# Optimization experiments

Hardware: AMD Instinct MI355X
Metric: run time of the kernel (lower is better)

The kernel has to match this reference:

```python
import jax, jax.numpy as jnp
import numpy as np

NEG_BIG = 1e20


def setup_inputs() -> dict:
    key = jax.random.key(0)
    k1, k2, k3 = jax.random.split(key, 3)
    B, Tenc, Tdec, D = 8, 2048, 512, 1024
    enc = jax.random.normal(k1, (B, Tenc, D), dtype=jnp.float32)
    dec = jax.random.normal(k2, (B, Tdec, D), dtype=jnp.float32)
    enc_mask = jax.random.randint(k3, (B, Tenc), 0, 2, dtype=jnp.int32)
    # guarantee at least one valid position per row to keep softmax well-defined
    enc_mask = enc_mask.at[:, 0].set(1)
    return {"enc": enc, "enc_mask": enc_mask, "dec": dec}


def reference(enc, enc_mask, dec):
    # dropout=0 and identity transforms -> enc_trans = enc, dec_trans = dec
    mask = enc_mask.astype(enc.dtype)  # (B, Tenc)
    # raw scores: sum_d dec[b,u,d] * enc[b,t,d] -> (B, Tenc, Tdec)
    raw = jnp.einsum('btd,bud->btu', enc, dec)
    raw = raw - (1.0 - mask)[:, :, None] * NEG_BIG
    scores = jax.nn.softmax(raw, axis=1)  # softmax over Tenc
    # context: sum_t scores[b,t,u] * enc[b,t,d] -> (B, Tdec, D)
    context = jnp.einsum('btu,btd->bud', scores, enc)
    return context, scores
```

## Files before the change

### kernel.cpp

```cpp
#include <hip/hip_runtime.h>
#include <math.h>

#define BATCH 8
#define TENC 2048
#define TDEC 512
#define DIM 1024
#define NEG_BIG 1e20f

typedef __attribute__((ext_vector_type(8))) short short8;
typedef __attribute__((ext_vector_type(4))) float f32x4;
typedef unsigned short ushort_t;

__device__ __forceinline__ unsigned int bf16rn(float x) {
    unsigned int u = __float_as_uint(x);
    return (u + 0x7FFFu + ((u >> 16) & 1u)) >> 16;
}
__device__ __forceinline__ float bf16f(unsigned int b) {
    return __uint_as_float(b << 16);
}
__device__ __forceinline__ void split2(float x, unsigned int& h, unsigned int& l) {
    h = bf16rn(x);
    l = bf16rn(x - bf16f(h));
}

#define GLOAD16(g, l)                                                        \
    __builtin_amdgcn_global_load_lds(                                        \
        (const __attribute__((address_space(1))) unsigned int*)(g),          \
        (__attribute__((address_space(3))) unsigned int*)(l), 16, 0, 0)


__global__ __launch_bounds__(256) void prep_enc(
    const float* __restrict__ enc, ushort_t* __restrict__ encH,
    ushort_t* __restrict__ encL, ushort_t* __restrict__ encT)
{
    __shared__ ushort_t T[64][72];

    const int b  = blockIdx.z;
    const int t0 = blockIdx.y * 64;
    const int d0 = blockIdx.x * 64;
    const int tid = threadIdx.x;

    const int tr = tid >> 4;
    const int dc = (tid & 15) * 4;

    const float* E = enc + (size_t)b * TENC * DIM;

#pragma unroll
    for (int i = 0; i < 4; ++i) {
        const int t = t0 + tr + 16 * i;
        float4 x = *(const float4*)&E[(size_t)t * DIM + d0 + dc];
        float xs[4] = {x.x, x.y, x.z, x.w};
        unsigned int h[4], l[4];
#pragma unroll
        for (int j = 0; j < 4; ++j) split2(xs[j], h[j], l[j]);
        ushort_t* ph = &encH[((size_t)b * TENC + t) * DIM + d0 + dc];
        ushort_t* pl = &encL[((size_t)b * TENC + t) * DIM + d0 + dc];
        *(uint2*)ph = make_uint2(h[0] | (h[1] << 16), h[2] | (h[3] << 16));
        *(uint2*)pl = make_uint2(l[0] | (l[1] << 16), l[2] | (l[3] << 16));
        const int tloc = tr + 16 * i;
#pragma unroll
        for (int j = 0; j < 4; ++j) T[dc + j][tloc] = (ushort_t)h[j];
    }
    __syncthreads();

    const int dr = tid >> 2;
    const int tc = (tid & 3) * 16;
    short8 v0 = *(const short8*)&T[dr][tc];
    short8 v1 = *(const short8*)&T[dr][tc + 8];
    ushort_t* out = &encT[((size_t)b * DIM + d0 + dr) * TENC + t0 + tc];
    *(short8*)out = v0;
    *(short8*)(out + 8) = v1;
}

__global__ __launch_bounds__(256) void prep_dec(
    const float* __restrict__ dec, ushort_t* __restrict__ decH,
    ushort_t* __restrict__ decL)
{
    const size_t i4 = (size_t)blockIdx.x * 256 + threadIdx.x;
    float4 x = *(const float4*)(dec + i4 * 4);
    float xs[4] = {x.x, x.y, x.z, x.w};
    unsigned int h[4], l[4];
#pragma unroll
    for (int j = 0; j < 4; ++j) split2(xs[j], h[j], l[j]);
    *(uint2*)(decH + i4 * 4) = make_uint2(h[0] | (h[1] << 16), h[2] | (h[3] << 16));
    *(uint2*)(decL + i4 * 4) = make_uint2(l[0] | (l[1] << 16), l[2] | (l[3] << 16));
}

__global__ __launch_bounds__(256) void gemm1_lds(
    const ushort_t* __restrict__ encH, const ushort_t* __restrict__ encL,
    const ushort_t* __restrict__ decH, const ushort_t* __restrict__ decL,
    const int* __restrict__ mask, float* __restrict__ raw,
    float* __restrict__ pm, float* __restrict__ ps)
{
    __shared__ __align__(16) ushort_t Ah[128 * 32];
    __shared__ __align__(16) ushort_t Al[128 * 32];
    __shared__ __align__(16) ushort_t Bh[128 * 32];
    __shared__ __align__(16) ushort_t Bl[128 * 32];
    __shared__ float smx[4][68];
    __shared__ float ssx[4][68];

    const int b  = blockIdx.z;
    const int m0 = blockIdx.y * 128;
    const int n0 = blockIdx.x * 128;
    const int tid = threadIdx.x;

    const int lane = tid & 63;
    const int w    = tid >> 6;
    const int wm   = (w & 1) * 64;
    const int wn   = (w >> 1) * 64;
    const int lr   = lane & 15;
    const int q    = lane >> 4;

    const int srow   = lane & 15;
    const int schunk = (lane >> 4) * 8;

    const int fa = wm * 32 + q * 128 + lr * 8;
    const int fb = wn * 32 + q * 128 + lr * 8;

    const ushort_t* AH = encH + (size_t)b * TENC * DIM;
    const ushort_t* AL = encL + (size_t)b * TENC * DIM;
    const ushort_t* BH = decH + (size_t)b * TDEC * DIM;
    const ushort_t* BL = decL + (size_t)b * TDEC * DIM;
    float* C = raw + (size_t)b * TENC * TDEC;

    f32x4 acc[4][4] = {};

    for (int k0 = 0; k0 < DIM; k0 += 32) {
        __syncthreads();
#pragma unroll
        for (int q2 = 0; q2 < 2; ++q2) {
            const int rg  = w * 2 + q2;
            const int row = rg * 16 + srow;
            const size_t ga = (size_t)(m0 + row) * DIM + k0 + schunk;
            const size_t gb = (size_t)(n0 + row) * DIM + k0 + schunk;
            GLOAD16(AH + ga, &Ah[rg * 512]);
            GLOAD16(AL + ga, &Al[rg * 512]);
            GLOAD16(BH + gb, &Bh[rg * 512]);
            GLOAD16(BL + gb, &Bl[rg * 512]);
        }
        __syncthreads();

        short8 ah[4], al[4], bh[4], bl[4];
#pragma unroll
        for (int i = 0; i < 4; ++i) {
            ah[i] = *(const short8*)&Ah[fa + i * 512];
            al[i] = *(const short8*)&Al[fa + i * 512];
            bh[i] = *(const short8*)&Bh[fb + i * 512];
            bl[i] = *(const short8*)&Bl[fb + i * 512];
        }
#pragma unroll
        for (int i = 0; i < 4; ++i)
#pragma unroll
            for (int j = 0; j < 4; ++j) {
                acc[i][j] = __builtin_amdgcn_mfma_f32_16x16x32_bf16(ah[i], bh[j], acc[i][j], 0, 0, 0);
                acc[i][j] = __builtin_amdgcn_mfma_f32_16x16x32_bf16(ah[i], bl[j], acc[i][j], 0, 0, 0);
                acc[i][j] = __builtin_amdgcn_mfma_f32_16x16x32_bf16(al[i], bh[j], acc[i][j], 0, 0, 0);
            }
    }

    float mkv[4][4];
#pragma unroll
    for (int i = 0; i < 4; ++i)
#pragma unroll
        for (int rr = 0; rr < 4; ++rr) {
            const int t = m0 + wm + i * 16 + q * 4 + rr;
            mkv[i][rr] = (mask[b * TENC + t] == 0) ? NEG_BIG : 0.0f;
        }

    float cm[4] = {-INFINITY, -INFINITY, -INFINITY, -INFINITY};
    float cs[4] = {0.f, 0.f, 0.f, 0.f};
#pragma unroll
    for (int i = 0; i < 4; ++i)
#pragma unroll
        for (int rr = 0; rr < 4; ++rr) {
            const int t = m0 + wm + i * 16 + q * 4 + rr;
#pragma unroll
            for (int j = 0; j < 4; ++j) {
                const int u = n0 + wn + j * 16 + lr;
                const float v = acc[i][j][rr] - mkv[i][rr];
                C[(size_t)t * TDEC + u] = v;
                cm[j] = fmaxf(cm[j], v);
            }
        }
#pragma unroll
    for (int i = 0; i < 4; ++i)
#pragma unroll
        for (int rr = 0; rr < 4; ++rr)
#pragma unroll
            for (int j = 0; j < 4; ++j)
                cs[j] += __expf(acc[i][j][rr] - mkv[i][rr] - cm[j]);

#pragma unroll
    for (int j = 0; j < 4; ++j) {
#pragma unroll
        for (int d = 16; d < 64; d <<= 1) {
            float om = __shfl_xor(cm[j], d, 64);
            float os = __shfl_xor(cs[j], d, 64);
            float mn = fmaxf(cm[j], om);
            cs[j] = cs[j] * __expf(cm[j] - mn) + os * __expf(om - mn);
            cm[j] = mn;
        }
    }

    if (q == 0) {
#pragma unroll
        for (int j = 0; j < 4; ++j) {
            smx[w][j * 16 + lr] = cm[j];
            ssx[w][j * 16 + lr] = cs[j];
        }
    }
    __syncthreads();
    if (tid < 128) {
        const int col = tid;
        const int wp  = (col >> 6) * 2;
        const int ci  = col & 63;
        const float m1 = smx[wp][ci],     s1 = ssx[wp][ci];
        const float m2 = smx[wp + 1][ci], s2 = ssx[wp + 1][ci];
        const float M = fmaxf(m1, m2);
        const float S = s1 * __expf(m1 - M) + s2 * __expf(m2 - M);
        const int idx = b * TDEC + n0 + col;
        const int tb  = m0 >> 7;
        pm[(size_t)tb * (BATCH * TDEC) + idx] = M;
        ps[(size_t)tb * (BATCH * TDEC) + idx] = S;
    }
}

__global__ __launch_bounds__(256) void colstat2(
    const float* __restrict__ pm, const float* __restrict__ ps,
    float* __restrict__ colM, float* __restrict__ colI)
{
    const int idx = blockIdx.x * 256 + threadIdx.x;
    float M = -INFINITY;
#pragma unroll
    for (int z = 0; z < 16; ++z)
        M = fmaxf(M, pm[(size_t)z * (BATCH * TDEC) + idx]);
    float s = 0.0f;
#pragma unroll
    for (int z = 0; z < 16; ++z)
        s += ps[(size_t)z * (BATCH * TDEC) + idx] *
             __expf(pm[(size_t)z * (BATCH * TDEC) + idx] - M);
    colM[idx] = M;
    colI[idx] = 1.0f / s;
}

__global__ __launch_bounds__(256) void norm_kernel(
    float* __restrict__ S, const float* __restrict__ colM,
    const float* __restrict__ colI, ushort_t* __restrict__ scoresT)
{
    __shared__ ushort_t T[64][72];

    const int b  = blockIdx.z;
    const int t0 = blockIdx.x * 64;
    const int u0 = blockIdx.y * 64;
    const int tid = threadIdx.x;

    const int tr  = tid >> 4;
    const int ucl = (tid & 15) * 4;

    float4 M4 = *(const float4*)&colM[b * TDEC + u0 + ucl];
    float4 I4 = *(const float4*)&colI[b * TDEC + u0 + ucl];

    float* base = S + (size_t)b * TENC * TDEC;

#pragma unroll
    for (int i = 0; i < 4; ++i) {
        const int t = t0 + tr + 16 * i;
        float4 x = *(const float4*)&base[(size_t)t * TDEC + u0 + ucl];
        float4 p;
        p.x = __expf(x.x - M4.x) * I4.x;
        p.y = __expf(x.y - M4.y) * I4.y;
        p.z = __expf(x.z - M4.z) * I4.z;
        p.w = __expf(x.w - M4.w) * I4.w;
        *(float4*)&base[(size_t)t * TDEC + u0 + ucl] = p;
        const int tloc = tr + 16 * i;
        T[ucl + 0][tloc] = (ushort_t)bf16rn(p.x);
        T[ucl + 1][tloc] = (ushort_t)bf16rn(p.y);
        T[ucl + 2][tloc] = (ushort_t)bf16rn(p.z);
        T[ucl + 3][tloc] = (ushort_t)bf16rn(p.w);
    }
    __syncthreads();

    const int ur = tid >> 2;
    const int tc = (tid & 3) * 16;
    short8 v0 = *(const short8*)&T[ur][tc];
    short8 v1 = *(const short8*)&T[ur][tc + 8];
    ushort_t* out = &scoresT[((size_t)b * TDEC + u0 + ur) * TENC + t0 + tc];
    *(short8*)out = v0;
    *(short8*)(out + 8) = v1;
}

__global__ __launch_bounds__(256) void gemm2_lds(
    const ushort_t* __restrict__ scoresT, const ushort_t* __restrict__ encT,
    float* __restrict__ p0, float* __restrict__ p1)
{
    __shared__ __align__(16) ushort_t Ah[128 * 32];
    __shared__ __align__(16) ushort_t Bh[128 * 32];

    const int b  = blockIdx.z >> 1;
    const int ks = blockIdx.z & 1;
    const int m0 = blockIdx.y * 128;
    const int n0 = blockIdx.x * 128;
    const int tid = threadIdx.x;

    const int lane = tid & 63;
    const int w    = tid >> 6;
    const int wm   = (w & 1) * 64;
    const int wn   = (w >> 1) * 64;
    const int lr   = lane & 15;
    const int q    = lane >> 4;

    const int srow   = lane & 15;
    const int schunk = (lane >> 4) * 8;
    const int fa = wm * 32 + q * 128 + lr * 8;
    const int fb = wn * 32 + q * 128 + lr * 8;

    const ushort_t* A = scoresT + (size_t)b * TDEC * TENC;
    const ushort_t* B = encT    + (size_t)b * DIM * TENC;
    float* P = (ks ? p1 : p0) + (size_t)b * TDEC * DIM;

    const int kbeg = ks * (TENC / 2);
    const int kend = kbeg + TENC / 2;

    f32x4 acc[4][4] = {};

    for (int k0 = kbeg; k0 < kend; k0 += 32) {
        __syncthreads();
#pragma unroll
        for (int q2 = 0; q2 < 2; ++q2) {
            const int rg  = w * 2 + q2;
            const int row = rg * 16 + srow;
            GLOAD16(A + (size_t)(m0 + row) * TENC + k0 + schunk, &Ah[rg * 512]);
            GLOAD16(B + (size_t)(n0 + row) * TENC + k0 + schunk, &Bh[rg * 512]);
        }
        __syncthreads();

        short8 ah[4], bh[4];
#pragma unroll
        for (int i = 0; i < 4; ++i) {
            ah[i] = *(const short8*)&Ah[fa + i * 512];
            bh[i] = *(const short8*)&Bh[fb + i * 512];
        }
#pragma unroll
        for (int i = 0; i < 4; ++i)
#pragma unroll
            for (int j = 0; j < 4; ++j)
                acc[i][j] = __builtin_amdgcn_mfma_f32_16x16x32_bf16(ah[i], bh[j], acc[i][j], 0, 0, 0);
    }

#pragma unroll
    for (int i = 0; i < 4; ++i)
#pragma unroll
        for (int rr = 0; rr < 4; ++rr) {
            const int u = m0 + wm + i * 16 + q * 4 + rr;
#pragma unroll
            for (int j = 0; j < 4; ++j) {
                const int d = n0 + wn + j * 16 + lr;
                P[(size_t)u * DIM + d] = acc[i][j][rr];
            }
        }
}

__global__ __launch_bounds__(256) void reduce_ctx(
    const float* __restrict__ p0, const float* __restrict__ p1,
    float* __restrict__ ctx)
{
    const size_t i4 = ((size_t)blockIdx.x * 256 + threadIdx.x) * 4;
    float4 a = *(const float4*)(p0 + i4);
    float4 b = *(const float4*)(p1 + i4);
    float4 o;
    o.x = a.x + b.x; o.y = a.y + b.y; o.z = a.z + b.z; o.w = a.w + b.w;
    *(float4*)(ctx + i4) = o;
}


__device__ __forceinline__ void store8(ushort_t* ph, ushort_t* pl,
                                       float4 x0, float4 x1) {
    float xs[8] = {x0.x, x0.y, x0.z, x0.w, x1.x, x1.y, x1.z, x1.w};
    short8 hv, lv;
#pragma unroll
    for (int i = 0; i < 8; ++i) {
        unsigned int h, l;
        split2(xs[i], h, l);
        hv[i] = (short)h;
        lv[i] = (short)l;
    }
    *(short8*)ph = hv;
    *(short8*)pl = lv;
}

__device__ __forceinline__ void wr4(ushort_t* ph, ushort_t* pl, const float* x) {
    unsigned int h[4], l[4];
#pragma unroll
    for (int i = 0; i < 4; ++i) split2(x[i], h[i], l[i]);
    *(uint2*)ph = make_uint2(h[0] | (h[1] << 16), h[2] | (h[3] << 16));
    *(uint2*)pl = make_uint2(l[0] | (l[1] << 16), l[2] | (l[3] << 16));
}

__device__ __forceinline__ short8 frag8B(const ushort_t* p) {
    union { short8 v; uint2 u[2]; } f;
    f.u[0] = *(const uint2*)p;
    f.u[1] = *(const uint2*)(p + 4);
    return f.v;
}

__global__ __launch_bounds__(256) void gemm1_mfma(
    const float* __restrict__ enc, const float* __restrict__ dec,
    const int* __restrict__ mask, float* __restrict__ raw)
{
    __shared__ __align__(16) ushort_t Ah[128 * 32];
    __shared__ __align__(16) ushort_t Al[128 * 32];
    __shared__ __align__(16) ushort_t Bh[128 * 32];
    __shared__ __align__(16) ushort_t Bl[128 * 32];

    const int b  = blockIdx.z;
    const int m0 = blockIdx.y * 128;
    const int n0 = blockIdx.x * 128;
    const int tid = threadIdx.x;

    const float* A  = enc + (size_t)b * TENC * DIM;
    const float* Bg = dec + (size_t)b * TDEC * DIM;
    float*       C  = raw + (size_t)b * TENC * TDEC;

    const int lane = tid & 63;
    const int wv   = tid >> 6;
    const int wm   = (wv & 1) * 64;
    const int wn   = (wv >> 1) * 64;
    const int lr   = lane & 15;
    const int q    = lane >> 4;

    const int r0 = tid >> 2;
    const int c8 = (tid & 3) * 8;

    f32x4 acc[4][4] = {};

    for (int k0 = 0; k0 < DIM; k0 += 32) {
        const float* pa0 = A  + (size_t)(m0 + r0) * DIM + k0 + c8;
        const float* pa1 = A  + (size_t)(m0 + r0 + 64) * DIM + k0 + c8;
        const float* pb0 = Bg + (size_t)(n0 + r0) * DIM + k0 + c8;
        const float* pb1 = Bg + (size_t)(n0 + r0 + 64) * DIM + k0 + c8;
        float4 a0 = *(const float4*)pa0, a0b = *(const float4*)(pa0 + 4);
        float4 a1 = *(const float4*)pa1, a1b = *(const float4*)(pa1 + 4);
        float4 b0 = *(const float4*)pb0, b0b = *(const float4*)(pb0 + 4);
        float4 b1 = *(const float4*)pb1, b1b = *(const float4*)(pb1 + 4);

        __syncthreads();
        store8(&Ah[r0 * 32 + c8],        &Al[r0 * 32 + c8],        a0, a0b);
        store8(&Ah[(r0 + 64) * 32 + c8], &Al[(r0 + 64) * 32 + c8], a1, a1b);
        store8(&Bh[r0 * 32 + c8],        &Bl[r0 * 32 + c8],        b0, b0b);
        store8(&Bh[(r0 + 64) * 32 + c8], &Bl[(r0 + 64) * 32 + c8], b1, b1b);
        __syncthreads();

        short8 ah[4], al[4], bh[4], bl[4];
#pragma unroll
        for (int i = 0; i < 4; ++i) {
            ah[i] = *(const short8*)&Ah[(wm + i * 16 + lr) * 32 + q * 8];
            al[i] = *(const short8*)&Al[(wm + i * 16 + lr) * 32 + q * 8];
            bh[i] = *(const short8*)&Bh[(wn + i * 16 + lr) * 32 + q * 8];
            bl[i] = *(const short8*)&Bl[(wn + i * 16 + lr) * 32 + q * 8];
        }
#pragma unroll
        for (int i = 0; i < 4; ++i)
#pragma unroll
            for (int j = 0; j < 4; ++j) {
                acc[i][j] = __builtin_amdgcn_mfma_f32_16x16x32_bf16(ah[i], bh[j], acc[i][j], 0, 0, 0);
                acc[i][j] = __builtin_amdgcn_mfma_f32_16x16x32_bf16(ah[i], bl[j], acc[i][j], 0, 0, 0);
                acc[i][j] = __builtin_amdgcn_mfma_f32_16x16x32_bf16(al[i], bh[j], acc[i][j], 0, 0, 0);
            }
    }

#pragma unroll
    for (int i = 0; i < 4; ++i)
#pragma unroll
        for (int rr = 0; rr < 4; ++rr) {
            const int t = m0 + wm + i * 16 + q * 4 + rr;
            const float mk = (mask[b * TENC + t] == 0) ? NEG_BIG : 0.0f;
#pragma unroll
            for (int j = 0; j < 4; ++j) {
                const int u = n0 + wn + j * 16 + lr;
                C[(size_t)t * TDEC + u] = acc[i][j][rr] - mk;
            }
        }
}

__global__ __launch_bounds__(256) void softmax_kernel(float* __restrict__ S)
{
    const int b  = blockIdx.y;
    const int u0 = blockIdx.x * 16;
    const int up = threadIdx.x & 15;
    const int tg = threadIdx.x >> 4;

    float* col = S + (size_t)b * TENC * TDEC + u0;

    float m = -INFINITY, s = 0.0f;
    for (int t = tg; t < TENC; t += 16) {
        float x = col[(size_t)t * TDEC + up];
        float mn = fmaxf(m, x);
        s = s * __expf(m - mn) + __expf(x - mn);
        m = mn;
    }

    __shared__ float sm[16][17];
    __shared__ float ss[16][17];
    sm[tg][up] = m;
    ss[tg][up] = s;
    __syncthreads();

    float M = -INFINITY;
#pragma unroll
    for (int j = 0; j < 16; ++j) M = fmaxf(M, sm[j][up]);
    float sum = 0.0f;
#pragma unroll
    for (int j = 0; j < 16; ++j) sum += ss[j][up] * __expf(sm[j][up] - M);
    const float inv = 1.0f / sum;

    for (int t = tg; t < TENC; t += 16) {
        float x = col[(size_t)t * TDEC + up];
        col[(size_t)t * TDEC + up] = __expf(x - M) * inv;
    }
}

#define G2_LD 36

__global__ __launch_bounds__(256) void gemm2_mfma(
    const float* __restrict__ scores, const float* __restrict__ enc,
    float* __restrict__ context)
{
    __shared__ __align__(16) ushort_t Ah[128 * G2_LD];
    __shared__ __align__(16) ushort_t Al[128 * G2_LD];
    __shared__ __align__(16) ushort_t Bh[128 * G2_LD];
    __shared__ __align__(16) ushort_t Bl[128 * G2_LD];

    const int b  = blockIdx.z;
    const int m0 = blockIdx.y * 128;
    const int n0 = blockIdx.x * 128;
    const int tid = threadIdx.x;

    const float* S = scores + (size_t)b * TENC * TDEC;
    const float* E = enc    + (size_t)b * TENC * DIM;
    float*       C = context + (size_t)b * TDEC * DIM;

    const int lane = tid & 63;
    const int wv   = tid >> 6;
    const int wm   = (wv & 1) * 64;
    const int wn   = (wv >> 1) * 64;
    const int lr   = lane & 15;
    const int q    = lane >> 4;

    const int ul = tid & 127;
    const int th = (tid >> 7) * 16;

    f32x4 acc[4][4] = {};

    for (int k0 = 0; k0 < TENC; k0 += 32) {
        float av[16], bv[16];
#pragma unroll
        for (int i = 0; i < 4; ++i) {
            const int t = k0 + th + i * 4;
#pragma unroll
            for (int j = 0; j < 4; ++j) {
                av[i * 4 + j] = S[(size_t)(t + j) * TDEC + m0 + ul];
                bv[i * 4 + j] = E[(size_t)(t + j) * DIM + n0 + ul];
            }
        }
        __syncthreads();
#pragma unroll
        for (int i = 0; i < 4; ++i) {
            const int tt = th + i * 4;
            wr4(&Ah[ul * G2_LD + tt], &Al[ul * G2_LD + tt], &av[i * 4]);
            wr4(&Bh[ul * G2_LD + tt], &Bl[ul * G2_LD + tt], &bv[i * 4]);
        }
        __syncthreads();

        short8 ah[4], al[4], bh[4], bl[4];
#pragma unroll
        for (int i = 0; i < 4; ++i) {
            ah[i] = frag8B(&Ah[(wm + i * 16 + lr) * G2_LD + q * 8]);
            al[i] = frag8B(&Al[(wm + i * 16 + lr) * G2_LD + q * 8]);
            bh[i] = frag8B(&Bh[(wn + i * 16 + lr) * G2_LD + q * 8]);
            bl[i] = frag8B(&Bl[(wn + i * 16 + lr) * G2_LD + q * 8]);
        }
#pragma unroll
        for (int i = 0; i < 4; ++i)
#pragma unroll
            for (int j = 0; j < 4; ++j) {
                acc[i][j] = __builtin_amdgcn_mfma_f32_16x16x32_bf16(ah[i], bh[j], acc[i][j], 0, 0, 0);
                acc[i][j] = __builtin_amdgcn_mfma_f32_16x16x32_bf16(ah[i], bl[j], acc[i][j], 0, 0, 0);
                acc[i][j] = __builtin_amdgcn_mfma_f32_16x16x32_bf16(al[i], bh[j], acc[i][j], 0, 0, 0);
            }
    }

#pragma unroll
    for (int i = 0; i < 4; ++i)
#pragma unroll
        for (int rr = 0; rr < 4; ++rr) {
            const int u = m0 + wm + i * 16 + q * 4 + rr;
#pragma unroll
            for (int j = 0; j < 4; ++j) {
                const int d = n0 + wn + j * 16 + lr;
                C[(size_t)u * DIM + d] = acc[i][j][rr];
            }
        }
}

extern "C" void kernel_launch(void* const* d_in, const int* in_sizes, int n_in,
                              void* d_out, int out_size, void* d_ws, size_t ws_size,
                              hipStream_t stream)
{
    const float* enc      = (const float*)d_in[0];
    const int*   enc_mask = (const int*)  d_in[1];
    const float* dec      = (const float*)d_in[2];

    float* context = (float*)d_out;
    float* scores  = context + (size_t)BATCH * TDEC * DIM;

    const size_t OFF_ENC_H = 0;
    const size_t OFF_ENC_L = 33554432;
    const size_t OFF_DEC_H = 67108864;
    const size_t OFF_DEC_L = 75497472;
    const size_t OFF_ENC_T = 83886080;
    const size_t OFF_SCO_T = 117440512;
    const size_t OFF_PM    = OFF_SCO_T;
    const size_t OFF_PS    = OFF_SCO_T + 262144;
    const size_t OFF_COL_M = 134217728;
    const size_t OFF_COL_I = 134234112;
    const size_t WS_NEED   = 134381568;

    if (ws_size >= WS_NEED) {
        char* w = (char*)d_ws;
        ushort_t* encH    = (ushort_t*)(w + OFF_ENC_H);
        ushort_t* encL    = (ushort_t*)(w + OFF_ENC_L);
        ushort_t* decH    = (ushort_t*)(w + OFF_DEC_H);
        ushort_t* decL    = (ushort_t*)(w + OFF_DEC_L);
        ushort_t* encT    = (ushort_t*)(w + OFF_ENC_T);
        ushort_t* scoresT = (ushort_t*)(w + OFF_SCO_T);
        float*    pm      = (float*)(w + OFF_PM);
        float*    ps      = (float*)(w + OFF_PS);
        float*    colM    = (float*)(w + OFF_COL_M);
        float*    colI    = (float*)(w + OFF_COL_I);
        float*    part0   = (float*)(w + OFF_ENC_H);
        float*    part1   = (float*)(w + OFF_ENC_L);

        prep_enc<<<dim3(DIM / 64, TENC / 64, BATCH), 256, 0, stream>>>(
            enc, encH, encL, encT);
        prep_dec<<<4096, 256, 0, stream>>>(dec, decH, decL);

        gemm1_lds<<<dim3(TDEC / 128, TENC / 128, BATCH), 256, 0, stream>>>(
            encH, encL, decH, decL, enc_mask, scores, pm, ps);

        colstat2<<<16, 256, 0, stream>>>(pm, ps, colM, colI);

        norm_kernel<<<dim3(TENC / 64, TDEC / 64, BATCH), 256, 0, stream>>>(
            scores, colM, colI, scoresT);

        gemm2_lds<<<dim3(DIM / 128, TDEC / 128, BATCH * 2), 256, 0, stream>>>(
            scoresT, encT, part0, part1);

        reduce_ctx<<<4096, 256, 0, stream>>>(part0, part1, context);
    } else {
        gemm1_mfma<<<dim3(TDEC / 128, TENC / 128, BATCH), 256, 0, stream>>>(
            enc, dec, enc_mask, scores);
        softmax_kernel<<<dim3(TDEC / 16, BATCH), 256, 0, stream>>>(scores);
        gemm2_mfma<<<dim3(DIM / 128, TDEC / 128, BATCH), 256, 0, stream>>>(
            scores, enc, context);
    }
}
```

Baseline: 271.5 us.

## Store bf16 operands in MFMA-tile-blocked layout for contiguous GEMM loads

The prep and normalization kernels now write the bf16 hi/lo splits of enc, dec, the transposed enc and the transposed scores into a blocked layout. Each 16-row by 32-k tile is stored as one contiguous 1 KB chunk. The GEMM kernels then fetch each 16x32 tile with one fully contiguous 1 KB global_load_lds per wave instead of 16 strided 64-byte row segments, which improves load coalescing and DRAM/TLB locality. In exchange, the prep kernels do scattered 16-byte writes and the layout is coupled to the tile shape.

```diff
diff --git a/kernel.cpp b/kernel.cpp
--- a/kernel.cpp
+++ b/kernel.cpp
@@ -28,6 +28,11 @@
         (const __attribute__((address_space(1))) unsigned int*)(g),          \
         (__attribute__((address_space(3))) unsigned int*)(l), 16, 0, 0)
 
+__device__ __forceinline__ size_t tiled_off(int row, int k, int ntK) {
+    return ((size_t)(row >> 4) * ntK + (k >> 5)) * 512
+         + ((k >> 3) & 3) * 128 + (row & 15) * 8;
+}
+
 
 __global__ __launch_bounds__(256) void prep_enc(
     const float* __restrict__ enc, ushort_t* __restrict__ encH,
@@ -40,50 +45,81 @@
     const int d0 = blockIdx.x * 64;
     const int tid = threadIdx.x;
 
-    const int tr = tid >> 4;
-    const int dc = (tid & 15) * 4;
-
     const float* E = enc + (size_t)b * TENC * DIM;
-
-#pragma unroll
-    for (int i = 0; i < 4; ++i) {
-        const int t = t0 + tr + 16 * i;
-        float4 x = *(const float4*)&E[(size_t)t * DIM + d0 + dc];
-        float xs[4] = {x.x, x.y, x.z, x.w};
-        unsigned int h[4], l[4];
-#pragma unroll
-        for (int j = 0; j < 4; ++j) split2(xs[j], h[j], l[j]);
-        ushort_t* ph = &encH[((size_t)b * TENC + t) * DIM + d0 + dc];
-        ushort_t* pl = &encL[((size_t)b * TENC + t) * DIM + d0 + dc];
-        *(uint2*)ph = make_uint2(h[0] | (h[1] << 16), h[2] | (h[3] << 16));
-        *(uint2*)pl = make_uint2(l[0] | (l[1] << 16), l[2] | (l[3] << 16));
-        const int tloc = tr + 16 * i;
-#pragma unroll
-        for (int j = 0; j < 4; ++j) T[dc + j][tloc] = (ushort_t)h[j];
+    const size_t bofs1 = (size_t)b * TENC * DIM;
+    const size_t bofs2 = (size_t)b * DIM * TENC;
+
+    const int ltr = tid >> 2;
+
+#pragma unroll
+    for (int it = 0; it < 2; ++it) {
+        const int c  = (tid & 3) + it * 4;
+        const int gt = t0 + ltr;
+        const int gd = d0 + c * 8;
+        float4 x0 = *(const float4*)&E[(size_t)gt * DIM + gd];
+        float4 x1 = *(const float4*)&E[(size_t)gt * DIM + gd + 4];
+        float xs[8] = {x0.x, x0.y, x0.z, x0.w, x1.x, x1.y, x1.z, x1.w};
+        unsigned int h[8], l[8];
+        short8 hv, lv;
+#pragma unroll
+        for (int j = 0; j < 8; ++j) {
+            split2(xs[j], h[j], l[j]);
+            hv[j] = (short)h[j];
+            lv[j] = (short)l[j];
+        }
+        const size_t off = bofs1 + tiled_off(gt, gd, DIM / 32);
+        *(short8*)&encH[off] = hv;
+        *(short8*)&encL[off] = lv;
+#pragma unroll
+        for (int j = 0; j < 8; ++j) T[c * 8 + j][ltr] = (ushort_t)h[j];
     }
     __syncthreads();
 
     const int dr = tid >> 2;
-    const int tc = (tid & 3) * 16;
-    short8 v0 = *(const short8*)&T[dr][tc];
-    short8 v1 = *(const short8*)&T[dr][tc + 8];
-    ushort_t* out = &encT[((size_t)b * DIM + d0 + dr) * TENC + t0 + tc];
-    *(short8*)out = v0;
-    *(short8*)(out + 8) = v1;
+#pragma unroll
+    for (int it = 0; it < 2; ++it) {
+        const int tc = (tid & 3) + it * 4;
+        const int gd = d0 + dr;
+        const int gt = t0 + tc * 8;
+        short8 v = *(const short8*)&T[dr][tc * 8];
+        *(short8*)&encT[bofs2 + tiled_off(gd, gt, TENC / 32)] = v;
+    }
 }
 
 __global__ __launch_bounds__(256) void prep_dec(
     const float* __restrict__ dec, ushort_t* __restrict__ decH,
     ushort_t* __restrict__ decL)
 {
-    const size_t i4 = (size_t)blockIdx.x * 256 + threadIdx.x;
-    float4 x = *(const float4*)(dec + i4 * 4);
-    float xs[4] = {x.x, x.y, x.z, x.w};
-    unsigned int h[4], l[4];
-#pragma unroll
-    for (int j = 0; j < 4; ++j) split2(xs[j], h[j], l[j]);
-    *(uint2*)(decH + i4 * 4) = make_uint2(h[0] | (h[1] << 16), h[2] | (h[3] << 16));
-    *(uint2*)(decL + i4 * 4) = make_uint2(l[0] | (l[1] << 16), l[2] | (l[3] << 16));
+    const int b  = blockIdx.z;
+    const int u0 = blockIdx.y * 64;
+    const int d0 = blockIdx.x * 64;
+    const int tid = threadIdx.x;
+
+    const float* D = dec + (size_t)b * TDEC * DIM;
+    const size_t bofs = (size_t)b * TDEC * DIM;
+
+    const int lur = tid >> 2;
+
+#pragma unroll
+    for (int it = 0; it < 2; ++it) {
+        const int c  = (tid & 3) + it * 4;
+        const int gu = u0 + lur;
+        const int gd = d0 + c * 8;
+        float4 x0 = *(const float4*)&D[(size_t)gu * DIM + gd];
+        float4 x1 = *(const float4*)&D[(size_t)gu * DIM + gd + 4];
+        float xs[8] = {x0.x, x0.y, x0.z, x0.w, x1.x, x1.y, x1.z, x1.w};
+        short8 hv, lv;
+#pragma unroll
+        for (int j = 0; j < 8; ++j) {
+            unsigned int h, l;
+            split2(xs[j], h, l);
+            hv[j] = (short)h;
+            lv[j] = (short)l;
+        }
+        const size_t off = bofs + tiled_off(gu, gd, DIM / 32);
+        *(short8*)&decH[off] = hv;
+        *(short8*)&decL[off] = lv;
+    }
 }
 
 __global__ __launch_bounds__(256) void gemm1_lds(
@@ -110,9 +146,7 @@
     const int wn   = (w >> 1) * 64;
     const int lr   = lane & 15;
     const int q    = lane >> 4;
-
-    const int srow   = lane & 15;
-    const int schunk = (lane >> 4) * 8;
+    const int l8   = lane * 8;
 
     const int fa = wm * 32 + q * 128 + lr * 8;
     const int fb = wn * 32 + q * 128 + lr * 8;
@@ -129,14 +163,13 @@
         __syncthreads();
 #pragma unroll
         for (int q2 = 0; q2 < 2; ++q2) {
-            const int rg  = w * 2 + q2;
-            const int row = rg * 16 + srow;
-            const size_t ga = (size_t)(m0 + row) * DIM + k0 + schunk;
-            const size_t gb = (size_t)(n0 + row) * DIM + k0 + schunk;
-            GLOAD16(AH + ga, &Ah[rg * 512]);
-            GLOAD16(AL + ga, &Al[rg * 512]);
-            GLOAD16(BH + gb, &Bh[rg * 512]);
-            GLOAD16(BL + gb, &Bl[rg * 512]);
+            const int rg = w * 2 + q2;
+            const size_t tA = ((size_t)((m0 >> 4) + rg) * (DIM / 32) + (k0 >> 5)) * 512 + l8;
+            const size_t tB = ((size_t)((n0 >> 4) + rg) * (DIM / 32) + (k0 >> 5)) * 512 + l8;
+            GLOAD16(AH + tA, &Ah[rg * 512]);
+            GLOAD16(AL + tA, &Al[rg * 512]);
+            GLOAD16(BH + tB, &Bh[rg * 512]);
+            GLOAD16(BL + tB, &Bl[rg * 512]);
         }
         __syncthreads();
 
@@ -280,13 +313,16 @@
     }
     __syncthreads();
 
+    const size_t bofs = (size_t)b * TDEC * TENC;
     const int ur = tid >> 2;
-    const int tc = (tid & 3) * 16;
-    short8 v0 = *(const short8*)&T[ur][tc];
-    short8 v1 = *(const short8*)&T[ur][tc + 8];
-    ushort_t* out = &scoresT[((size_t)b * TDEC + u0 + ur) * TENC + t0 + tc];
-    *(short8*)out = v0;
-    *(short8*)(out + 8) = v1;
+#pragma unroll
+    for (int it = 0; it < 2; ++it) {
+        const int tc = (tid & 3) + it * 4;
+        const int gu = u0 + ur;
+        const int gt = t0 + tc * 8;
+        short8 v = *(const short8*)&T[ur][tc * 8];
+        *(short8*)&scoresT[bofs + tiled_off(gu, gt, TENC / 32)] = v;
+    }
 }
 
 __global__ __launch_bounds__(256) void gemm2_lds(
@@ -308,9 +344,8 @@
     const int wn   = (w >> 1) * 64;
     const int lr   = lane & 15;
     const int q    = lane >> 4;
-
-    const int srow   = lane & 15;
-    const int schunk = (lane >> 4) * 8;
+    const int l8   = lane * 8;
+
     const int fa = wm * 32 + q * 128 + lr * 8;
     const int fb = wn * 32 + q * 128 + lr * 8;
 
@@ -327,10 +362,11 @@
         __syncthreads();
 #pragma unroll
         for (int q2 = 0; q2 < 2; ++q2) {
-            const int rg  = w * 2 + q2;
-            const int row = rg * 16 + srow;
-            GLOAD16(A + (size_t)(m0 + row) * TENC + k0 + schunk, &Ah[rg * 512]);
-            GLOAD16(B + (size_t)(n0 + row) * TENC + k0 + schunk, &Bh[rg * 512]);
+            const int rg = w * 2 + q2;
+            const size_t tA = ((size_t)((m0 >> 4) + rg) * (TENC / 32) + (k0 >> 5)) * 512 + l8;
+            const size_t tB = ((size_t)((n0 >> 4) + rg) * (TENC / 32) + (k0 >> 5)) * 512 + l8;
+            GLOAD16(A + tA, &Ah[rg * 512]);
+            GLOAD16(B + tB, &Bh[rg * 512]);
         }
         __syncthreads();
 
@@ -642,7 +678,8 @@
 
         prep_enc<<<dim3(DIM / 64, TENC / 64, BATCH), 256, 0, stream>>>(
             enc, encH, encL, encT);
-        prep_dec<<<4096, 256, 0, stream>>>(dec, decH, decL);
+        prep_dec<<<dim3(DIM / 64, TDEC / 64, BATCH), 256, 0, stream>>>(
+            dec, decH, decL);
 
         gemm1_lds<<<dim3(TDEC / 128, TENC / 128, BATCH), 256, 0, stream>>>(
             encH, encL, decH, decL, enc_mask, scores, pm, ps);
```

After: 240.0 us. 1.13x faster.
